# Kernel tuning notes

Measured on AMD Instinct MI355X. Metric: run time of the kernel, lower is better.

Reference implementation:

```python
import jax, jax.numpy as jnp
import numpy as np

B = 16384      # batch
H = 512        # experts_hidden
E = 5          # num_experts
T = 2          # num_tasks
OUT = 128      # fixed protein expert output width (from .view(-1, E, 1, 128))


def setup_inputs() -> dict:
    key = jax.random.key(0)
    ks = jax.random.split(key, 12)
    s = 0.02  # init scale
    return {
        "share_x": jax.random.normal(ks[0], (B, H), jnp.float32),
        "task_x0": jax.random.normal(ks[1], (B, H), jnp.float32),
        "task_x1": jax.random.normal(ks[2], (B, H), jnp.float32),
        # shared experts: stacked weights for all E experts
        "share_W1": jax.random.normal(ks[3], (E, H, H), jnp.float32) * s,
        "share_b1": jnp.zeros((E, H), jnp.float32),
        "share_W2": jax.random.normal(ks[4], (E, H, OUT), jnp.float32) * s,
        "share_b2": jnp.zeros((E, OUT), jnp.float32),
        # task experts: [T, E, ...]
        "task_W1": jax.random.normal(ks[5], (T, E, H, H), jnp.float32) * s,
        "task_b1": jnp.zeros((T, E, H), jnp.float32),
        "task_W2": jax.random.normal(ks[6], (T, E, H, OUT), jnp.float32) * s,
        "task_b2": jnp.zeros((T, E, OUT), jnp.float32),
    }


def _expert_bank(x, W1, b1, W2, b2):
    """Run all E experts on x in one batched GEMM pair.

    x: [B, H]; W1: [E, H, H]; W2: [E, H, OUT].
    Equivalent to torch.concat([e(x) for e in experts], dim=0)
    followed by .view(-1, E, 1, OUT).
    """
    h = jax.nn.relu(jnp.einsum('bh,ehk->ebk', x, W1) + b1[:, None, :])  # [E,B,H]
    o = jnp.einsum('ebk,eko->ebo', h, W2) + b2[:, None, :]              # [E,B,OUT]
    # concat along dim 0 == flatten (E,B) -> E*B, then view(-1, E, 1, OUT)
    return o.reshape(-1, E, 1, OUT)


def reference(share_x, task_x0, task_x1,
              share_W1, share_b1, share_W2, share_b2,
              task_W1, task_b1, task_W2, task_b2):
    share_out = _expert_bank(share_x, share_W1, share_b1, share_W2, share_b2)
    task_xs = (task_x0, task_x1)
    task_outs = tuple(
        _expert_bank(task_xs[i], task_W1[i], task_b1[i], task_W2[i], task_b2[i])
        for i in range(T)
    )
    return (share_out,) + task_outs
```

## Files before the change

kernel.cpp:

```cpp
#include <hip/hip_runtime.h>

#define H 512
#define OW 128
#define NB 16384

typedef float f32x4 __attribute__((ext_vector_type(4)));
typedef short short8 __attribute__((ext_vector_type(8)));
typedef unsigned short ushort8v __attribute__((ext_vector_type(8)));

static __device__ __forceinline__ unsigned short f2bf(float f) {
    union { float f; unsigned u; } v; v.f = f;
    return (unsigned short)((v.u + 0x7FFFu + ((v.u >> 16) & 1u)) >> 16);
}

static __device__ __forceinline__ f32x4 mfma16(short8 a, short8 b, f32x4 c) {
    return __builtin_amdgcn_mfma_f32_16x16x32_bf16(a, b, c, 0, 0, 0);
}

static __device__ __forceinline__ void sw_write(unsigned short* l, int row, int ch, ushort8v v) {
    *(ushort8v*)&l[row * 64 + ((ch ^ (row & 7)) << 3)] = v;
}
static __device__ __forceinline__ short8 sw_read(const unsigned short* l, int row, int ch) {
    return *(const short8*)&l[row * 64 + ((ch ^ (row & 7)) << 3)];
}

__global__ void prep_w1(const float* __restrict__ share_W1,
                        const float* __restrict__ task_W1,
                        unsigned short* __restrict__ w1t) {
    const int inst = blockIdx.z;
    const float* src = (inst < 5) ? (share_W1 + (size_t)inst * H * H)
                                  : (task_W1 + (size_t)(inst - 5) * H * H);
    unsigned short* dst = w1t + (size_t)inst * H * H;
    const int g = blockIdx.x * 256 + threadIdx.x;
    const int n = g & (H - 1);
    const int kc = g >> 9;
    float v[8];
#pragma unroll
    for (int i = 0; i < 8; ++i) v[i] = src[(size_t)(kc * 8 + i) * H + n];
    ushort8v o;
#pragma unroll
    for (int i = 0; i < 8; ++i) o[i] = f2bf(v[i]);
    *(ushort8v*)&dst[(size_t)n * H + kc * 8] = o;
}

__global__ void prep_w2(const float* __restrict__ share_W2,
                        const float* __restrict__ task_W2,
                        unsigned short* __restrict__ w2t) {
    const int inst = blockIdx.z;
    const float* src = (inst < 5) ? (share_W2 + (size_t)inst * H * OW)
                                  : (task_W2 + (size_t)(inst - 5) * H * OW);
    unsigned short* dst = w2t + (size_t)inst * OW * H;
    const int g = blockIdx.x * 256 + threadIdx.x;
    const int n = g & (OW - 1);
    const int kc = g >> 7;
    float v[8];
#pragma unroll
    for (int i = 0; i < 8; ++i) v[i] = src[(size_t)(kc * 8 + i) * OW + n];
    ushort8v o;
#pragma unroll
    for (int i = 0; i < 8; ++i) o[i] = f2bf(v[i]);
    *(ushort8v*)&dst[(size_t)n * H + kc * 8] = o;
}

__global__ void prep_x(const float* __restrict__ x0, const float* __restrict__ x1,
                       const float* __restrict__ x2, unsigned short* __restrict__ xb) {
    const int z = blockIdx.z;
    const float* s = (z == 0) ? x0 : (z == 1 ? x1 : x2);
    const size_t g = (size_t)(blockIdx.x * 256 + threadIdx.x) * 8;
    float4 a = *(const float4*)&s[g];
    float4 b = *(const float4*)&s[g + 4];
    ushort8v o;
    o[0] = f2bf(a.x); o[1] = f2bf(a.y); o[2] = f2bf(a.z); o[3] = f2bf(a.w);
    o[4] = f2bf(b.x); o[5] = f2bf(b.y); o[6] = f2bf(b.z); o[7] = f2bf(b.w);
    *(ushort8v*)&xb[(size_t)z * NB * H + g] = o;
}

__global__ __launch_bounds__(256, 3) void gemm1(
    const unsigned short* __restrict__ xb, const unsigned short* __restrict__ w1t,
    const float* __restrict__ share_b1, const float* __restrict__ task_b1,
    unsigned short* __restrict__ hbuf, int z)
{
    __shared__ unsigned short smem[128 * 136];
    unsigned short* sA  = smem;
    unsigned short* sBt = smem + 8192;
    unsigned short* sH  = smem;

    const int tid = threadIdx.x;
    const int lane = tid & 63;
    const int wave = tid >> 6;
    const int wy = wave >> 1, wx = wave & 1;
    const int lm = lane & 15, lq = lane >> 4;
    const int r8 = tid >> 3, ch = tid & 7;

    const int bid = blockIdx.x;
    const int e = bid % 5;
    const int nt = (bid / 5) & 3;
    const int rowtile = bid / 20;
    const int inst = z * 5 + e;

    const unsigned short* xp = xb + ((size_t)z * NB + rowtile * 128) * H;
    const unsigned short* wp = w1t + (size_t)inst * H * H + (size_t)(nt * 128) * H;
    const float* b1 = (z == 0) ? (share_b1 + e * H) : (task_b1 + ((z - 1) * 5 + e) * H);
    unsigned short* hp = hbuf + ((size_t)e * NB + rowtile * 128) * H + nt * 128;

    ushort8v rA[4], rB[4];
#pragma unroll
    for (int it = 0; it < 4; ++it) {
        rA[it] = *(const ushort8v*)&xp[(size_t)(it * 32 + r8) * H + ch * 8];
        rB[it] = *(const ushort8v*)&wp[(size_t)(it * 32 + r8) * H + ch * 8];
    }

    const f32x4 z4 = {0.f, 0.f, 0.f, 0.f};
    f32x4 acc[4][4];
#pragma unroll
    for (int i = 0; i < 4; ++i)
#pragma unroll
        for (int j = 0; j < 4; ++j) acc[i][j] = z4;

    for (int kt = 0; kt < 8; ++kt) {
        __syncthreads();
#pragma unroll
        for (int it = 0; it < 4; ++it) sw_write(sA, it * 32 + r8, ch, rA[it]);
#pragma unroll
        for (int it = 0; it < 4; ++it) sw_write(sBt, it * 32 + r8, ch, rB[it]);
        __syncthreads();
        if (kt < 7) {
            const int k0 = (kt + 1) * 64;
#pragma unroll
            for (int it = 0; it < 4; ++it) {
                rA[it] = *(const ushort8v*)&xp[(size_t)(it * 32 + r8) * H + k0 + ch * 8];
                rB[it] = *(const ushort8v*)&wp[(size_t)(it * 32 + r8) * H + k0 + ch * 8];
            }
        }
#pragma unroll
        for (int kk = 0; kk < 2; ++kk) {
            short8 af[4], bf[4];
#pragma unroll
            for (int i = 0; i < 4; ++i) af[i] = sw_read(sA, wy * 64 + i * 16 + lm, kk * 4 + lq);
#pragma unroll
            for (int j = 0; j < 4; ++j) bf[j] = sw_read(sBt, wx * 64 + j * 16 + lm, kk * 4 + lq);
#pragma unroll
            for (int i = 0; i < 4; ++i)
#pragma unroll
                for (int j = 0; j < 4; ++j) acc[i][j] = mfma16(af[i], bf[j], acc[i][j]);
        }
    }

    __syncthreads();
#pragma unroll
    for (int j = 0; j < 4; ++j) {
        const int col = wx * 64 + j * 16 + lm;
        const float b1v = b1[nt * 128 + col];
#pragma unroll
        for (int i = 0; i < 4; ++i)
#pragma unroll
            for (int r = 0; r < 4; ++r) {
                const int row = wy * 64 + i * 16 + lq * 4 + r;
                sH[row * 136 + col] = f2bf(fmaxf(acc[i][j][r] + b1v, 0.f));
            }
    }
    __syncthreads();
    {
        const int rr = tid >> 4, cc = tid & 15;
#pragma unroll
        for (int it = 0; it < 8; ++it) {
            const int row = rr + it * 16;
            ushort8v v = *(const ushort8v*)&sH[row * 136 + cc * 8];
            *(ushort8v*)&hp[(size_t)row * H + cc * 8] = v;
        }
    }
}

__global__ __launch_bounds__(256, 4) void gemm2(
    const unsigned short* __restrict__ hbuf, const unsigned short* __restrict__ w2t,
    const float* __restrict__ share_b2, const float* __restrict__ task_b2,
    float* __restrict__ out, int z)
{
    __shared__ unsigned short smem[4096 + 8192];
    unsigned short* sH  = smem;
    unsigned short* sW2 = smem + 4096;

    const int tid = threadIdx.x;
    const int lane = tid & 63;
    const int wave = tid >> 6;
    const int wy = wave >> 1, wx = wave & 1;
    const int lm = lane & 15, lq = lane >> 4;
    const int r8 = tid >> 3, ch = tid & 7;

    const int bid = blockIdx.x;
    const int e = bid % 5;
    const int rt = bid / 5;
    const int inst = z * 5 + e;

    const unsigned short* hp = hbuf + ((size_t)e * NB + rt * 64) * H;
    const unsigned short* wp = w2t + (size_t)inst * OW * H;
    const float* b2 = (z == 0) ? (share_b2 + e * OW) : (task_b2 + ((z - 1) * 5 + e) * OW);
    float* op = out + ((size_t)inst * NB + rt * 64) * OW;

    ushort8v rH[2], rW[4];
#pragma unroll
    for (int it = 0; it < 2; ++it)
        rH[it] = *(const ushort8v*)&hp[(size_t)(it * 32 + r8) * H + ch * 8];
#pragma unroll
    for (int it = 0; it < 4; ++it)
        rW[it] = *(const ushort8v*)&wp[(size_t)(it * 32 + r8) * H + ch * 8];

    const f32x4 z4 = {0.f, 0.f, 0.f, 0.f};
    f32x4 acc[2][4];
#pragma unroll
    for (int i = 0; i < 2; ++i)
#pragma unroll
        for (int j = 0; j < 4; ++j) acc[i][j] = z4;

    for (int kt = 0; kt < 8; ++kt) {
        __syncthreads();
#pragma unroll
        for (int it = 0; it < 2; ++it) sw_write(sH, it * 32 + r8, ch, rH[it]);
#pragma unroll
        for (int it = 0; it < 4; ++it) sw_write(sW2, it * 32 + r8, ch, rW[it]);
        __syncthreads();
        if (kt < 7) {
            const int k0 = (kt + 1) * 64;
#pragma unroll
            for (int it = 0; it < 2; ++it)
                rH[it] = *(const ushort8v*)&hp[(size_t)(it * 32 + r8) * H + k0 + ch * 8];
#pragma unroll
            for (int it = 0; it < 4; ++it)
                rW[it] = *(const ushort8v*)&wp[(size_t)(it * 32 + r8) * H + k0 + ch * 8];
        }
#pragma unroll
        for (int kk = 0; kk < 2; ++kk) {
            short8 af[2], bf[4];
#pragma unroll
            for (int i = 0; i < 2; ++i) af[i] = sw_read(sH, wy * 32 + i * 16 + lm, kk * 4 + lq);
#pragma unroll
            for (int j = 0; j < 4; ++j) bf[j] = sw_read(sW2, wx * 64 + j * 16 + lm, kk * 4 + lq);
#pragma unroll
            for (int i = 0; i < 2; ++i)
#pragma unroll
                for (int j = 0; j < 4; ++j) acc[i][j] = mfma16(af[i], bf[j], acc[i][j]);
        }
    }

#pragma unroll
    for (int j = 0; j < 4; ++j) {
        const int col = wx * 64 + j * 16 + lm;
        const float b2v = b2[col];
#pragma unroll
        for (int i = 0; i < 2; ++i)
#pragma unroll
            for (int r = 0; r < 4; ++r) {
                const int row = wy * 32 + i * 16 + lq * 4 + r;
                op[(size_t)row * OW + col] = acc[i][j][r] + b2v;
            }
    }
}

extern "C" void kernel_launch(void* const* d_in, const int* in_sizes, int n_in,
                              void* d_out, int out_size, void* d_ws, size_t ws_size,
                              hipStream_t stream) {
    const float* share_x  = (const float*)d_in[0];
    const float* task_x0  = (const float*)d_in[1];
    const float* task_x1  = (const float*)d_in[2];
    const float* share_W1 = (const float*)d_in[3];
    const float* share_b1 = (const float*)d_in[4];
    const float* share_W2 = (const float*)d_in[5];
    const float* share_b2 = (const float*)d_in[6];
    const float* task_W1  = (const float*)d_in[7];
    const float* task_b1  = (const float*)d_in[8];
    const float* task_W2  = (const float*)d_in[9];
    const float* task_b2  = (const float*)d_in[10];
    float* out = (float*)d_out;

    unsigned short* w1t  = (unsigned short*)d_ws;
    unsigned short* w2t  = w1t + (size_t)15 * H * H;
    unsigned short* xb   = w2t + (size_t)15 * OW * H;
    unsigned short* hbuf = xb + (size_t)3 * NB * H;

    prep_w1<<<dim3(128, 1, 15), 256, 0, stream>>>(share_W1, task_W1, w1t);
    prep_w2<<<dim3(32, 1, 15), 256, 0, stream>>>(share_W2, task_W2, w2t);
    prep_x <<<dim3(4096, 1, 3), 256, 0, stream>>>(share_x, task_x0, task_x1, xb);
    for (int z = 0; z < 3; ++z) {
        gemm1<<<2560, 256, 0, stream>>>(xb, w1t, share_b1, task_b1, hbuf, z);
        gemm2<<<1280, 256, 0, stream>>>(hbuf, w2t, share_b2, task_b2, out, z);
    }
}
```

Measured before the change: 444.7 us.

## Fuse both expert GEMMs into one kernel keeping hidden activations in LDS

Replaces the six per-bank gemm1/gemm2 launches with a single fused kernel. Each block computes a 128-row tile of the hidden layer in 128-column chunks, applies bias and ReLU into LDS, and immediately accumulates the second GEMM, so the bf16 hidden buffer never goes to global memory. It also remaps block indices so neighbouring blocks share expert weights. The cost is more LDS per block, lower occupancy (launch bounds 2), the X tile re-read for every N chunk, and fewer total blocks (1920).

```diff
diff --git a/kernel.cpp b/kernel.cpp
--- a/kernel.cpp
+++ b/kernel.cpp
@@ -75,15 +75,19 @@
     *(ushort8v*)&xb[(size_t)z * NB * H + g] = o;
 }
 
-__global__ __launch_bounds__(256, 3) void gemm1(
+__global__ __launch_bounds__(256, 2) void fused(
     const unsigned short* __restrict__ xb, const unsigned short* __restrict__ w1t,
+    const unsigned short* __restrict__ w2t,
     const float* __restrict__ share_b1, const float* __restrict__ task_b1,
-    unsigned short* __restrict__ hbuf, int z)
+    const float* __restrict__ share_b2, const float* __restrict__ task_b2,
+    float* __restrict__ out)
 {
-    __shared__ unsigned short smem[128 * 136];
+    __shared__ unsigned short smem[33792];
     unsigned short* sA  = smem;
-    unsigned short* sBt = smem + 8192;
-    unsigned short* sH  = smem;
+    unsigned short* sB  = smem + 8192;
+    unsigned short* sH  = smem + 16384;
+    unsigned short* sW0 = smem;
+    unsigned short* sW1 = smem + 8192;
 
     const int tid = threadIdx.x;
     const int lane = tid & 63;
@@ -92,153 +96,123 @@
     const int lm = lane & 15, lq = lane >> 4;
     const int r8 = tid >> 3, ch = tid & 7;
 
-    const int bid = blockIdx.x;
-    const int e = bid % 5;
-    const int nt = (bid / 5) & 3;
-    const int rowtile = bid / 20;
+    const int swz = (blockIdx.x & 7) * 240 + (blockIdx.x >> 3);
+    const int z = swz / 640;
+    const int rzi = swz % 640;
+    const int rowtile = rzi / 5;
+    const int e = rzi % 5;
     const int inst = z * 5 + e;
 
-    const unsigned short* xp = xb + ((size_t)z * NB + rowtile * 128) * H;
-    const unsigned short* wp = w1t + (size_t)inst * H * H + (size_t)(nt * 128) * H;
+    const unsigned short* xp  = xb + ((size_t)z * NB + rowtile * 128) * H;
+    const unsigned short* w1p = w1t + (size_t)inst * H * H;
+    const unsigned short* w2p = w2t + (size_t)inst * OW * H;
     const float* b1 = (z == 0) ? (share_b1 + e * H) : (task_b1 + ((z - 1) * 5 + e) * H);
-    unsigned short* hp = hbuf + ((size_t)e * NB + rowtile * 128) * H + nt * 128;
+    const float* b2 = (z == 0) ? (share_b2 + e * OW) : (task_b2 + ((z - 1) * 5 + e) * OW);
+    float* op = out + ((size_t)inst * NB + rowtile * 128) * OW;
+
+    const f32x4 zero4 = {0.f, 0.f, 0.f, 0.f};
+    f32x4 acc2[4][4];
+#pragma unroll
+    for (int i = 0; i < 4; ++i)
+#pragma unroll
+        for (int j = 0; j < 4; ++j) acc2[i][j] = zero4;
 
     ushort8v rA[4], rB[4];
 #pragma unroll
     for (int it = 0; it < 4; ++it) {
         rA[it] = *(const ushort8v*)&xp[(size_t)(it * 32 + r8) * H + ch * 8];
-        rB[it] = *(const ushort8v*)&wp[(size_t)(it * 32 + r8) * H + ch * 8];
+        rB[it] = *(const ushort8v*)&w1p[(size_t)(it * 32 + r8) * H + ch * 8];
     }
 
-    const f32x4 z4 = {0.f, 0.f, 0.f, 0.f};
-    f32x4 acc[4][4];
-#pragma unroll
-    for (int i = 0; i < 4; ++i)
-#pragma unroll
-        for (int j = 0; j < 4; ++j) acc[i][j] = z4;
-
-    for (int kt = 0; kt < 8; ++kt) {
+    for (int nt = 0; nt < 4; ++nt) {
+        const unsigned short* wnp = w1p + (size_t)(nt * 128) * H;
+
+        f32x4 acc1[4][4];
+#pragma unroll
+        for (int i = 0; i < 4; ++i)
+#pragma unroll
+            for (int j = 0; j < 4; ++j) acc1[i][j] = zero4;
+
+        for (int kt = 0; kt < 8; ++kt) {
+            __syncthreads();
+#pragma unroll
+            for (int it = 0; it < 4; ++it) sw_write(sA, it * 32 + r8, ch, rA[it]);
+#pragma unroll
+            for (int it = 0; it < 4; ++it) sw_write(sB, it * 32 + r8, ch, rB[it]);
+            __syncthreads();
+            if (kt < 7) {
+                const int k0 = (kt + 1) * 64;
+#pragma unroll
+                for (int it = 0; it < 4; ++it) {
+                    rA[it] = *(const ushort8v*)&xp[(size_t)(it * 32 + r8) * H + k0 + ch * 8];
+                    rB[it] = *(const ushort8v*)&wnp[(size_t)(it * 32 + r8) * H + k0 + ch * 8];
+                }
+            }
+#pragma unroll
+            for (int kk = 0; kk < 2; ++kk) {
+                short8 af[4], bfr[4];
+#pragma unroll
+                for (int i = 0; i < 4; ++i) af[i] = sw_read(sA, wy * 64 + i * 16 + lm, kk * 4 + lq);
+#pragma unroll
+                for (int j = 0; j < 4; ++j) bfr[j] = sw_read(sB, wx * 64 + j * 16 + lm, kk * 4 + lq);
+#pragma unroll
+                for (int i = 0; i < 4; ++i)
+#pragma unroll
+                    for (int j = 0; j < 4; ++j) acc1[i][j] = mfma16(af[i], bfr[j], acc1[i][j]);
+            }
+        }
         __syncthreads();
-#pragma unroll
-        for (int it = 0; it < 4; ++it) sw_write(sA, it * 32 + r8, ch, rA[it]);
-#pragma unroll
-        for (int it = 0; it < 4; ++it) sw_write(sBt, it * 32 + r8, ch, rB[it]);
+
+        ushort8v rW[4][2];
+#pragma unroll
+        for (int it = 0; it < 4; ++it) {
+            const size_t wb = (size_t)(it * 32 + r8) * H + nt * 128 + ch * 8;
+            rW[it][0] = *(const ushort8v*)&w2p[wb];
+            rW[it][1] = *(const ushort8v*)&w2p[wb + 64];
+        }
+
+#pragma unroll
+        for (int j = 0; j < 4; ++j) {
+            const int col = wx * 64 + j * 16 + lm;
+            const float b1v = b1[nt * 128 + col];
+#pragma unroll
+            for (int i = 0; i < 4; ++i)
+#pragma unroll
+                for (int rr = 0; rr < 4; ++rr) {
+                    const int row = wy * 64 + i * 16 + lq * 4 + rr;
+                    sH[row * 136 + col] = f2bf(fmaxf(acc1[i][j][rr] + b1v, 0.f));
+                }
+        }
+
+#pragma unroll
+        for (int it = 0; it < 4; ++it) {
+            sw_write(sW0, it * 32 + r8, ch, rW[it][0]);
+            sw_write(sW1, it * 32 + r8, ch, rW[it][1]);
+        }
+
+        if (nt < 3) {
+            const unsigned short* wn2 = w1p + (size_t)((nt + 1) * 128) * H;
+#pragma unroll
+            for (int it = 0; it < 4; ++it) {
+                rA[it] = *(const ushort8v*)&xp[(size_t)(it * 32 + r8) * H + ch * 8];
+                rB[it] = *(const ushort8v*)&wn2[(size_t)(it * 32 + r8) * H + ch * 8];
+            }
+        }
         __syncthreads();
-        if (kt < 7) {
-            const int k0 = (kt + 1) * 64;
-#pragma unroll
-            for (int it = 0; it < 4; ++it) {
-                rA[it] = *(const ushort8v*)&xp[(size_t)(it * 32 + r8) * H + k0 + ch * 8];
-                rB[it] = *(const ushort8v*)&wp[(size_t)(it * 32 + r8) * H + k0 + ch * 8];
-            }
-        }
-#pragma unroll
-        for (int kk = 0; kk < 2; ++kk) {
-            short8 af[4], bf[4];
-#pragma unroll
-            for (int i = 0; i < 4; ++i) af[i] = sw_read(sA, wy * 64 + i * 16 + lm, kk * 4 + lq);
-#pragma unroll
-            for (int j = 0; j < 4; ++j) bf[j] = sw_read(sBt, wx * 64 + j * 16 + lm, kk * 4 + lq);
+
+#pragma unroll
+        for (int kk = 0; kk < 4; ++kk) {
+            short8 af[4], bfr[4];
 #pragma unroll
             for (int i = 0; i < 4; ++i)
-#pragma unroll
-                for (int j = 0; j < 4; ++j) acc[i][j] = mfma16(af[i], bf[j], acc[i][j]);
-        }
-    }
-
-    __syncthreads();
-#pragma unroll
-    for (int j = 0; j < 4; ++j) {
-        const int col = wx * 64 + j * 16 + lm;
-        const float b1v = b1[nt * 128 + col];
-#pragma unroll
-        for (int i = 0; i < 4; ++i)
-#pragma unroll
-            for (int r = 0; r < 4; ++r) {
-                const int row = wy * 64 + i * 16 + lq * 4 + r;
-                sH[row * 136 + col] = f2bf(fmaxf(acc[i][j][r] + b1v, 0.f));
-            }
-    }
-    __syncthreads();
-    {
-        const int rr = tid >> 4, cc = tid & 15;
-#pragma unroll
-        for (int it = 0; it < 8; ++it) {
-            const int row = rr + it * 16;
-            ushort8v v = *(const ushort8v*)&sH[row * 136 + cc * 8];
-            *(ushort8v*)&hp[(size_t)row * H + cc * 8] = v;
-        }
-    }
-}
-
-__global__ __launch_bounds__(256, 4) void gemm2(
-    const unsigned short* __restrict__ hbuf, const unsigned short* __restrict__ w2t,
-    const float* __restrict__ share_b2, const float* __restrict__ task_b2,
-    float* __restrict__ out, int z)
-{
-    __shared__ unsigned short smem[4096 + 8192];
-    unsigned short* sH  = smem;
-    unsigned short* sW2 = smem + 4096;
-
-    const int tid = threadIdx.x;
-    const int lane = tid & 63;
-    const int wave = tid >> 6;
-    const int wy = wave >> 1, wx = wave & 1;
-    const int lm = lane & 15, lq = lane >> 4;
-    const int r8 = tid >> 3, ch = tid & 7;
-
-    const int bid = blockIdx.x;
-    const int e = bid % 5;
-    const int rt = bid / 5;
-    const int inst = z * 5 + e;
-
-    const unsigned short* hp = hbuf + ((size_t)e * NB + rt * 64) * H;
-    const unsigned short* wp = w2t + (size_t)inst * OW * H;
-    const float* b2 = (z == 0) ? (share_b2 + e * OW) : (task_b2 + ((z - 1) * 5 + e) * OW);
-    float* op = out + ((size_t)inst * NB + rt * 64) * OW;
-
-    ushort8v rH[2], rW[4];
-#pragma unroll
-    for (int it = 0; it < 2; ++it)
-        rH[it] = *(const ushort8v*)&hp[(size_t)(it * 32 + r8) * H + ch * 8];
-#pragma unroll
-    for (int it = 0; it < 4; ++it)
-        rW[it] = *(const ushort8v*)&wp[(size_t)(it * 32 + r8) * H + ch * 8];
-
-    const f32x4 z4 = {0.f, 0.f, 0.f, 0.f};
-    f32x4 acc[2][4];
-#pragma unroll
-    for (int i = 0; i < 2; ++i)
-#pragma unroll
-        for (int j = 0; j < 4; ++j) acc[i][j] = z4;
-
-    for (int kt = 0; kt < 8; ++kt) {
-        __syncthreads();
-#pragma unroll
-        for (int it = 0; it < 2; ++it) sw_write(sH, it * 32 + r8, ch, rH[it]);
-#pragma unroll
-        for (int it = 0; it < 4; ++it) sw_write(sW2, it * 32 + r8, ch, rW[it]);
-        __syncthreads();
-        if (kt < 7) {
-            const int k0 = (kt + 1) * 64;
-#pragma unroll
-            for (int it = 0; it < 2; ++it)
-                rH[it] = *(const ushort8v*)&hp[(size_t)(it * 32 + r8) * H + k0 + ch * 8];
-#pragma unroll
-            for (int it = 0; it < 4; ++it)
-                rW[it] = *(const ushort8v*)&wp[(size_t)(it * 32 + r8) * H + k0 + ch * 8];
-        }
-#pragma unroll
-        for (int kk = 0; kk < 2; ++kk) {
-            short8 af[2], bf[4];
-#pragma unroll
-            for (int i = 0; i < 2; ++i) af[i] = sw_read(sH, wy * 32 + i * 16 + lm, kk * 4 + lq);
-#pragma unroll
-            for (int j = 0; j < 4; ++j) bf[j] = sw_read(sW2, wx * 64 + j * 16 + lm, kk * 4 + lq);
-#pragma unroll
-            for (int i = 0; i < 2; ++i)
-#pragma unroll
-                for (int j = 0; j < 4; ++j) acc[i][j] = mfma16(af[i], bf[j], acc[i][j]);
+                af[i] = *(const short8*)&sH[(wy * 64 + i * 16 + lm) * 136 + kk * 32 + lq * 8];
+#pragma unroll
+            for (int j = 0; j < 4; ++j)
+                bfr[j] = sw_read((kk & 2) ? sW1 : sW0, wx * 64 + j * 16 + lm, (kk & 1) * 4 + lq);
+#pragma unroll
+            for (int i = 0; i < 4; ++i)
+#pragma unroll
+                for (int j = 0; j < 4; ++j) acc2[i][j] = mfma16(af[i], bfr[j], acc2[i][j]);
         }
     }
 
@@ -247,11 +221,11 @@
         const int col = wx * 64 + j * 16 + lm;
         const float b2v = b2[col];
 #pragma unroll
-        for (int i = 0; i < 2; ++i)
-#pragma unroll
-            for (int r = 0; r < 4; ++r) {
-                const int row = wy * 32 + i * 16 + lq * 4 + r;
-                op[(size_t)row * OW + col] = acc[i][j][r] + b2v;
+        for (int i = 0; i < 4; ++i)
+#pragma unroll
+            for (int rr = 0; rr < 4; ++rr) {
+                const int row = wy * 64 + i * 16 + lq * 4 + rr;
+                op[(size_t)row * OW + col] = acc2[i][j][rr] + b2v;
             }
     }
 }
@@ -272,16 +246,13 @@
     const float* task_b2  = (const float*)d_in[10];
     float* out = (float*)d_out;
 
-    unsigned short* w1t  = (unsigned short*)d_ws;
-    unsigned short* w2t  = w1t + (size_t)15 * H * H;
-    unsigned short* xb   = w2t + (size_t)15 * OW * H;
-    unsigned short* hbuf = xb + (size_t)3 * NB * H;
+    unsigned short* w1t = (unsigned short*)d_ws;
+    unsigned short* w2t = w1t + (size_t)15 * H * H;
+    unsigned short* xb  = w2t + (size_t)15 * OW * H;
 
     prep_w1<<<dim3(128, 1, 15), 256, 0, stream>>>(share_W1, task_W1, w1t);
     prep_w2<<<dim3(32, 1, 15), 256, 0, stream>>>(share_W2, task_W2, w2t);
     prep_x <<<dim3(4096, 1, 3), 256, 0, stream>>>(share_x, task_x0, task_x1, xb);
-    for (int z = 0; z < 3; ++z) {
-        gemm1<<<2560, 256, 0, stream>>>(xb, w1t, share_b1, task_b1, hbuf, z);
-        gemm2<<<1280, 256, 0, stream>>>(hbuf, w2t, share_b2, task_b2, out, z);
-    }
-}
+    fused<<<1920, 256, 0, stream>>>(xb, w1t, w2t, share_b1, task_b1,
+                                    share_b2, task_b2, out);
+}
```

Result: no change. 436.5 us (-1.8%).
